# Kernel optimization log

Hardware: AMD Instinct MI355X
Metric: run time of the kernel (lower is better)

Reference implementation:

```python
import jax, jax.numpy as jnp
import numpy as np

# ---- static config (mirrors init_kwargs) ----
NS, NV, ORDER = 16, 4, 1
NUM_RBF, NUM_CH = 8, 4
C = NUM_RBF * NUM_CH              # 32 output channels per l in out_irreps
N_NODES, N_EDGES = 10000, 128000
NODE_FEAT, EDGE_FEAT = 64, 16
RDIM, RMAX = 32, 12.0
L, FC_DIM = 2, 64
# FullyConnectedTensorProduct weight numel for order=1 paths:
# (0x0->0), (0x1->1), (1x0->1), (1x1->0), (1x1->1)
WNUM = NS*NS + NS*NV + NV*NV + NV*NS + NV*NV  # 416


def _get_sorter(order, nc):
    # faithful port of TensorProductConvModel.get_sorter
    idx, orl = [], []
    for l in range(order + 1):
        for n in range(nc):
            idx.extend([n] * (2 * l + 1))
            orl.extend(range(l * l, (l + 1) * (l + 1)))
    idx, orl = np.array(idx), np.array(orl)
    return np.argsort(idx * (orl.max() + 1) + orl, kind='stable')

SORTER = jnp.asarray(_get_sorter(ORDER, C))


def _mlp(x, W1, b1, W2, b2):
    return jnp.maximum(x @ W1 + b1, 0.0) @ W2 + b2


def setup_inputs() -> dict:
    key = jax.random.key(0)
    ks = jax.random.split(key, 24)
    rn = lambda k, sh, sc: jax.random.normal(k, sh, dtype=jnp.float32) * sc
    s = lambda f: 1.0 / np.sqrt(f)
    inp = {}
    inp['pos'] = rn(ks[0], (N_NODES, 3), 3.0)
    inp['node_feats'] = rn(ks[1], (N_NODES, NODE_FEAT), 1.0)
    inp['edge_attr_in'] = rn(ks[2], (N_EDGES, EDGE_FEAT), 1.0)
    inp['edge_index'] = jax.random.randint(ks[3], (2, N_EDGES), 0, N_NODES)
    # Encoder (linear) + node_embedding MLP
    inp['enc_W'] = rn(ks[4], (NODE_FEAT, NS), s(NODE_FEAT)); inp['enc_b'] = jnp.zeros((NS,), jnp.float32)
    inp['ne_W1'] = rn(ks[5], (NS, NS), s(NS)); inp['ne_b1'] = jnp.zeros((NS,), jnp.float32)
    inp['ne_W2'] = rn(ks[6], (NS, NS), s(NS)); inp['ne_b2'] = jnp.zeros((NS,), jnp.float32)
    # edge_embedding MLP
    inp['ee_W1'] = rn(ks[7], (EDGE_FEAT, NS), s(EDGE_FEAT)); inp['ee_b1'] = jnp.zeros((NS,), jnp.float32)
    inp['ee_W2'] = rn(ks[8], (NS, NS), s(NS)); inp['ee_b2'] = jnp.zeros((NS,), jnp.float32)
    # radius_embedding MLP
    inp['re_W1'] = rn(ks[9], (RDIM, NS), s(RDIM)); inp['re_b1'] = jnp.zeros((NS,), jnp.float32)
    inp['re_W2'] = rn(ks[10], (NS, NS), s(NS)); inp['re_b2'] = jnp.zeros((NS,), jnp.float32)
    # per-layer TP edge-weight MLPs (stacked over L layers)
    inp['fc1_W'] = rn(ks[11], (L, 3 * NS, FC_DIM), s(3 * NS)); inp['fc1_b'] = jnp.zeros((L, FC_DIM), jnp.float32)
    inp['fc2_W'] = rn(ks[12], (L, FC_DIM, WNUM), s(FC_DIM)); inp['fc2_b'] = jnp.zeros((L, WNUM), jnp.float32)
    # final o3.Linear (per-l channel mixing)
    inp['lin0_W'] = rn(ks[13], (NS, C), 1.0)
    inp['lin1_W'] = rn(ks[14], (NV, C), 1.0)
    return inp


def _forward(pos, node_feats, edge_attr_in, enc_W, enc_b, ne_W1, ne_b1, ne_W2, ne_b2,
             ee_W1, ee_b1, ee_W2, ee_b2, re_W1, re_b1, re_W2, re_b2,
             fc1_W, fc1_b, fc2_W, fc2_b, lin0_W, lin1_W, edge_index):
    src, dst = edge_index[0], edge_index[1]
    N, E = pos.shape[0], src.shape[0]
    # node scalar features: Encoder -> node_embedding MLP
    h0 = _mlp(node_feats @ enc_W + enc_b, ne_W1, ne_b1, ne_W2, ne_b2)        # [N, ns]
    h1 = jnp.zeros((N, NV, 3), h0.dtype)                                      # l=1 part (zero-padded)
    # build_conv_graph (radius=False): given edges only
    edge_vec = pos[src] - pos[dst]                                            # [E, 3]
    d = jnp.linalg.norm(edge_vec, axis=-1)
    offset = jnp.linspace(0.0, RMAX, RDIM)
    coeff = -0.5 / (offset[1] - offset[0]) ** 2
    rbf = jnp.exp(coeff * (d[:, None] - offset[None, :]) ** 2)                # GaussianSmearing
    edge_attr = _mlp(edge_attr_in, ee_W1, ee_b1, ee_W2, ee_b2) + _mlp(rbf, re_W1, re_b1, re_W2, re_b2)
    # spherical harmonics, normalize=True, component normalization: Y0=1, Y1=sqrt(3)*unit
    unit = edge_vec / jnp.maximum(d, 1e-9)[:, None]
    y1 = jnp.sqrt(3.0) * unit                                                 # [E, 3]
    # scatter-mean denominators (dim_size = N)
    cnt = jnp.maximum(jax.ops.segment_sum(jnp.ones((E,), h0.dtype), src, num_segments=N), 1.0)
    a0 = 1.0 / jnp.sqrt(float(NS + NV))       # path (fan-in) norm for l=0 output
    a1 = 1.0 / jnp.sqrt(float(NS + 2 * NV))   # path norm for l=1 output
    for i in range(L):
        # edge features: [edge_attr | h0[src] | h0[dst]] -> per-edge TP weights
        ea = jnp.concatenate([edge_attr, h0[src], h0[dst]], -1)
        w = _mlp(ea, fc1_W[i], fc1_b[i], fc2_W[i], fc2_b[i])                  # [E, WNUM]
        off = 0
        w00 = w[:, off:off + NS * NS].reshape(E, NS, NS); off += NS * NS
        w011 = w[:, off:off + NS * NV].reshape(E, NS, NV); off += NS * NV
        w101 = w[:, off:off + NV * NV].reshape(E, NV, NV); off += NV * NV
        w110 = w[:, off:off + NV * NS].reshape(E, NV, NS); off += NV * NS
        w111 = w[:, off:off + NV * NV].reshape(E, NV, NV)
        x0, x1 = h0[dst], h1[dst]                                             # gather at edge_dst
        # l=0 output: (0x0->0) + (1x1->0)
        dot = jnp.einsum('enk,ek->en', x1, y1) / jnp.sqrt(3.0)
        o0 = a0 * (jnp.einsum('en,eno->eo', x0, w00) + jnp.einsum('en,eno->eo', dot, w110))
        # l=1 output: (0x1->1) + (1x0->1) + (1x1->1 cross)
        cr = jnp.cross(x1, y1[:, None, :]) / jnp.sqrt(2.0)                    # [E, nv, 3]
        o1 = a1 * (jnp.einsum('en,eno,em->eom', x0, w011, y1)
                   + jnp.einsum('enm,eno->eom', x1, w101)
                   + jnp.einsum('enm,eno->eom', cr, w111))
        # scatter-mean into edge_src, residual add
        h0 = h0 + jax.ops.segment_sum(o0, src, num_segments=N) / cnt[:, None]
        h1 = h1 + jax.ops.segment_sum(o1.reshape(E, -1), src, num_segments=N).reshape(N, NV, 3) / cnt[:, None, None]
    # final o3.Linear (per-l, fan-in normalized) -> sorter -> reshape
    f0 = (h0 @ lin0_W) / jnp.sqrt(float(NS))                                   # [N, C]
    f1 = jnp.einsum('nvm,vc->ncm', h1, lin1_W) / jnp.sqrt(float(NV))           # [N, C, 3]
    flat = jnp.concatenate([f0, f1.reshape(N, C * 3)], -1)                     # irreps-flat layout
    return flat[:, SORTER].reshape(N, NUM_CH, NUM_RBF, (ORDER + 1) ** 2)


def reference(pos, node_feats, edge_attr_in, edge_index, enc_W, enc_b, ne_W1, ne_b1, ne_W2, ne_b2,
              ee_W1, ee_b1, ee_W2, ee_b2, re_W1, re_b1, re_W2, re_b2,
              fc1_W, fc1_b, fc2_W, fc2_b, lin0_W, lin1_W):
    return _forward(pos, node_feats, edge_attr_in, enc_W, enc_b, ne_W1, ne_b1, ne_W2, ne_b2,
                    ee_W1, ee_b1, ee_W2, ee_b2, re_W1, re_b1, re_W2, re_b2,
                    fc1_W, fc1_b, fc2_W, fc2_b, lin0_W, lin1_W, edge_index)
```

## Files before the change

kernel.cpp:

```cpp
#include <hip/hip_runtime.h>
#include <math.h>

#define SQRT3f     1.7320508075688772f
#define INV_SQRT3f 0.5773502691896258f
#define INV_SQRT2f 0.7071067811865476f
#define A0f        0.22360679774997896f
#define A1f        0.20412414523193150f

typedef __attribute__((ext_vector_type(8))) short bf16x8;
typedef __attribute__((ext_vector_type(4))) float f32x4;

__device__ __forceinline__ float4 ld4(const float* p) {
    return *reinterpret_cast<const float4*>(p);
}

__device__ __forceinline__ unsigned short f2bf(float x) {
    unsigned int u = __float_as_uint(x);
    u = (u + 0x7FFFu + ((u >> 16) & 1u)) >> 16;
    return (unsigned short)u;
}
__device__ __forceinline__ float bf2f(unsigned short u) {
    return __uint_as_float(((unsigned int)u) << 16);
}
__device__ __forceinline__ unsigned int pk2(float a, float b) {
    return (unsigned int)f2bf(a) | ((unsigned int)f2bf(b) << 16);
}
__device__ __forceinline__ float bflo(unsigned int u) {
    return __uint_as_float(u << 16);
}
__device__ __forceinline__ float bfhi(unsigned int u) {
    return __uint_as_float(u & 0xFFFF0000u);
}
__device__ __forceinline__ float pick4(uint2 v, int r) {
    return (r == 0) ? bflo(v.x) : (r == 1) ? bfhi(v.x)
         : (r == 2) ? bflo(v.y) : bfhi(v.y);
}

template<bool RELU>
__device__ __forceinline__ void mm16x16(const float* in, const float* W,
                                        const float* b, float* out)
{
#pragma unroll
    for (int t = 0; t < 16; ++t) out[t] = b[t];
#pragma unroll
    for (int s = 0; s < 16; ++s) {
        float a = in[s];
#pragma unroll
        for (int q = 0; q < 4; ++q) {
            float4 w = *reinterpret_cast<const float4*>(W + s * 16 + q * 4);
            out[q*4+0] += a * w.x; out[q*4+1] += a * w.y;
            out[q*4+2] += a * w.z; out[q*4+3] += a * w.w;
        }
    }
    if (RELU) {
#pragma unroll
        for (int t = 0; t < 16; ++t) out[t] = fmaxf(out[t], 0.f);
    }
}

__global__ __launch_bounds__(256)
void embed_hist_pack_kernel(const float* __restrict__ nf,
                            const float* __restrict__ encW, const float* __restrict__ encb,
                            const float* __restrict__ neW1, const float* __restrict__ neb1,
                            const float* __restrict__ neW2, const float* __restrict__ neb2,
                            float* __restrict__ h0, int N,
                            const int* __restrict__ srcI, int* __restrict__ cntI, int E,
                            const float* __restrict__ fc2W, const float* __restrict__ fc1W,
                            unsigned short* __restrict__ w2p, unsigned short* __restrict__ w1p,
                            int nblkA, int nblkB)
{
    int tid = threadIdx.x;
    int bid = (int)blockIdx.x;
    if (bid >= nblkA + nblkB) {
        int idx = (bid - nblkA - nblkB) * 256 + tid;
        const int NW2 = 2 * 26 * 2 * 64;
        if (idx < NW2) {
            int lane  = idx & 63;
            int ks    = (idx >> 6) & 1;
            int nt    = (idx >> 7) % 26;
            int layer = idx / (26 * 2 * 64);
            const float* W = fc2W + (size_t)layer * 64 * 416;
            unsigned short* out = w2p + (size_t)layer * 26 * 2 * 64 * 8
                                      + (size_t)((nt * 2 + ks) * 64 + lane) * 8;
            int k0 = ks * 32 + (lane >> 4) * 8;
            int c  = nt * 16 + (lane & 15);
#pragma unroll
            for (int j = 0; j < 8; ++j) out[j] = f2bf(W[(size_t)(k0 + j) * 416 + c]);
        } else {
            int i2 = idx - NW2;
            if (i2 >= 2 * 4 * 2 * 64) return;
            int lane  = i2 & 63;
            int ks    = (i2 >> 6) & 1;
            int nt    = (i2 >> 7) & 3;
            int layer = i2 >> 9;
            const float* W = fc1W + (size_t)layer * 48 * 64;
            unsigned short* out = w1p + (size_t)(((layer * 4 + nt) * 2 + ks) * 64 + lane) * 8;
            int k0 = ks * 32 + (lane >> 4) * 8;
            int n  = nt * 16 + (lane & 15);
#pragma unroll
            for (int j = 0; j < 8; ++j) {
                int k = k0 + j;
                out[j] = (k < 48) ? f2bf(W[(size_t)k * 64 + n]) : (unsigned short)0;
            }
        }
        return;
    }
    if (bid >= nblkA) {
        int e = (bid - nblkA) * 256 + tid;
        if (e < E) atomicAdd(&cntI[srcI[e]], 1);
        return;
    }
    __shared__ float encWs[1024];
    __shared__ float neW1s[256];
    __shared__ float neW2s[256];
    __shared__ float bs[48];
    for (int i = tid; i < 1024; i += 256) encWs[i] = encW[i];
    neW1s[tid] = neW1[tid];
    neW2s[tid] = neW2[tid];
    if (tid < 16)      bs[tid] = encb[tid];
    else if (tid < 32) bs[tid] = neb1[tid - 16];
    else if (tid < 48) bs[tid] = neb2[tid - 32];
    __syncthreads();

    int n = bid * 256 + tid;
    if (n >= N) return;
    float x[16];
#pragma unroll
    for (int s = 0; s < 16; ++s) x[s] = bs[s];
    for (int i = 0; i < 64; ++i) {
        float a = nf[(size_t)n * 64 + i];
#pragma unroll
        for (int q = 0; q < 4; ++q) {
            float4 w = *reinterpret_cast<const float4*>(&encWs[i * 16 + q * 4]);
            x[q*4+0] += a * w.x; x[q*4+1] += a * w.y;
            x[q*4+2] += a * w.z; x[q*4+3] += a * w.w;
        }
    }
    float h[16], o[16];
    mm16x16<true >(x, neW1s, bs + 16, h);
    mm16x16<false>(h, neW2s, bs + 32, o);
#pragma unroll
    for (int j = 0; j < 16; ++j) h0[(size_t)n * 16 + j] = o[j];
}

__global__ __launch_bounds__(1024)
void scan_kernel(const int* __restrict__ cntI, int* __restrict__ start,
                 int* __restrict__ cursor, float* __restrict__ invcnt, int N)
{
    __shared__ int wsum[16];
    __shared__ int ctot;
    int tid = threadIdx.x;
    int lane = tid & 63, wid = tid >> 6;
    int run = 0;
    for (int c0 = 0; c0 < N; c0 += 1024) {
        int i = c0 + tid;
        int v = (i < N) ? cntI[i] : 0;
        int x = v;
#pragma unroll
        for (int off = 1; off < 64; off <<= 1) {
            int y = __shfl_up(x, off);
            if (lane >= off) x += y;
        }
        if (lane == 63) wsum[wid] = x;
        __syncthreads();
        if (wid == 0) {
            int w = (lane < 16) ? wsum[lane] : 0;
#pragma unroll
            for (int off = 1; off < 16; off <<= 1) {
                int y = __shfl_up(w, off);
                if (lane >= off) w += y;
            }
            if (lane < 16) wsum[lane] = w;
            if (lane == 15) ctot = w;
        }
        __syncthreads();
        int base = (wid > 0) ? wsum[wid - 1] : 0;
        int incl = x + base;
        if (i < N) {
            int st = run + incl - v;
            start[i] = st;
            cursor[i] = st;
            invcnt[i] = 1.0f / fmaxf((float)v, 1.0f);
        }
        run += ctot;
        __syncthreads();
    }
}

__global__ __launch_bounds__(256)
void edge_pre_kernel(const float* __restrict__ pos, const float* __restrict__ eain,
                     const int* __restrict__ srcI, const int* __restrict__ dstI,
                     int* __restrict__ cursor,
                     const float* __restrict__ eeW1, const float* __restrict__ eeb1,
                     const float* __restrict__ eeW2, const float* __restrict__ eeb2,
                     const float* __restrict__ reW1, const float* __restrict__ reb1,
                     const float* __restrict__ reW2, const float* __restrict__ reb2,
                     float* __restrict__ eattr, float* __restrict__ y1s,
                     int* __restrict__ srcS, int* __restrict__ dstS, int E)
{
    __shared__ float ws_[1280];
    __shared__ float bs_[64];
    float* eeW1s = ws_;
    float* eeW2s = ws_ + 256;
    float* reW1s = ws_ + 512;
    float* reW2s = ws_ + 1024;
    int tid = threadIdx.x;
    eeW1s[tid] = eeW1[tid];
    eeW2s[tid] = eeW2[tid];
    reW1s[tid] = reW1[tid];
    reW1s[tid + 256] = reW1[tid + 256];
    reW2s[tid] = reW2[tid];
    if (tid < 16)      bs_[tid] = eeb1[tid];
    else if (tid < 32) bs_[tid] = eeb2[tid - 16];
    else if (tid < 48) bs_[tid] = reb1[tid - 32];
    else if (tid < 64) bs_[tid] = reb2[tid - 48];
    __syncthreads();

    int e = blockIdx.x * blockDim.x + tid;
    if (e >= E) return;
    int s = srcI[e], d = dstI[e];
    int p = atomicAdd(&cursor[s], 1);
    srcS[p] = s; dstS[p] = d;
    float vx = pos[s*3+0] - pos[d*3+0];
    float vy = pos[s*3+1] - pos[d*3+1];
    float vz = pos[s*3+2] - pos[d*3+2];
    float dist = sqrtf(vx*vx + vy*vy + vz*vz);
    float inv = 1.f / fmaxf(dist, 1e-9f);
    y1s[(size_t)p*3+0] = SQRT3f * vx * inv;
    y1s[(size_t)p*3+1] = SQRT3f * vy * inv;
    y1s[(size_t)p*3+2] = SQRT3f * vz * inv;

    const float step  = 12.0f / 31.0f;
    const float coeff = -0.5f / (step * step);
    float rbf[32];
#pragma unroll
    for (int j = 0; j < 32; ++j) {
        float t = dist - (float)j * step;
        rbf[j] = expf(coeff * t * t);
    }

    float ein[16];
#pragma unroll
    for (int j = 0; j < 16; ++j) ein[j] = eain[(size_t)e * 16 + j];

    float t1[16], a1v[16];
    mm16x16<true >(ein, eeW1s, bs_, t1);
    mm16x16<false>(t1, eeW2s, bs_ + 16, a1v);

    float t2[16];
#pragma unroll
    for (int t = 0; t < 16; ++t) t2[t] = bs_[32 + t];
#pragma unroll
    for (int j = 0; j < 32; ++j) {
        float a = rbf[j];
#pragma unroll
        for (int q = 0; q < 4; ++q) {
            float4 w = *reinterpret_cast<const float4*>(&reW1s[j * 16 + q * 4]);
            t2[q*4+0] += a * w.x; t2[q*4+1] += a * w.y;
            t2[q*4+2] += a * w.z; t2[q*4+3] += a * w.w;
        }
    }
#pragma unroll
    for (int t = 0; t < 16; ++t) t2[t] = fmaxf(t2[t], 0.f);
    float a2v[16];
    mm16x16<false>(t2, reW2s, bs_ + 48, a2v);

#pragma unroll
    for (int j = 0; j < 16; ++j) eattr[(size_t)p * 16 + j] = a1v[j] + a2v[j];
}

template<bool HAS_L1>
__global__ __launch_bounds__(256)
void fused_tp_kernel(const float* __restrict__ h0, const float* __restrict__ h1,
                     const float* __restrict__ eattr, const float* __restrict__ y1s,
                     const int* __restrict__ srcS, const int* __restrict__ dstS,
                     const unsigned short* __restrict__ w1p, const float* __restrict__ b1,
                     const unsigned short* __restrict__ w2p, const float* __restrict__ b2,
                     float* __restrict__ oo0, float* __restrict__ oo1, int E)
{
    __shared__ unsigned short eas[128 * 64];
    __shared__ unsigned short x0sT[16 * 128];
    __shared__ unsigned short x1sT[12 * 128];
    __shared__ unsigned short dotsT[4 * 128];
    __shared__ unsigned short crsT[12 * 128];
    __shared__ unsigned short y1lT[3 * 128];

    int tid = threadIdx.x;
    int ebase = blockIdx.x * 128;

    {
        int lx = tid & 127;
        int half = tid >> 7;
        int p = ebase + lx;
        int sw = lx & 7;
        uint4 pk;
        if (half == 0) {
            float4 va = ld4(eattr + (size_t)p * 16 + 0);
            float4 vb = ld4(eattr + (size_t)p * 16 + 4);
            float4 vc = ld4(eattr + (size_t)p * 16 + 8);
            float4 vd = ld4(eattr + (size_t)p * 16 + 12);
            pk.x = pk2(va.x, va.y); pk.y = pk2(va.z, va.w);
            pk.z = pk2(vb.x, vb.y); pk.w = pk2(vb.z, vb.w);
            *reinterpret_cast<uint4*>(&eas[lx * 64 + ((0 ^ sw) << 3)]) = pk;
            pk.x = pk2(vc.x, vc.y); pk.y = pk2(vc.z, vc.w);
            pk.z = pk2(vd.x, vd.y); pk.w = pk2(vd.z, vd.w);
            *reinterpret_cast<uint4*>(&eas[lx * 64 + ((1 ^ sw) << 3)]) = pk;

            int s = srcS[p];
            va = ld4(h0 + (size_t)s * 16 + 0); vb = ld4(h0 + (size_t)s * 16 + 4);
            vc = ld4(h0 + (size_t)s * 16 + 8); vd = ld4(h0 + (size_t)s * 16 + 12);
            pk.x = pk2(va.x, va.y); pk.y = pk2(va.z, va.w);
            pk.z = pk2(vb.x, vb.y); pk.w = pk2(vb.z, vb.w);
            *reinterpret_cast<uint4*>(&eas[lx * 64 + ((2 ^ sw) << 3)]) = pk;
            pk.x = pk2(vc.x, vc.y); pk.y = pk2(vc.z, vc.w);
            pk.z = pk2(vd.x, vd.y); pk.w = pk2(vd.z, vd.w);
            *reinterpret_cast<uint4*>(&eas[lx * 64 + ((3 ^ sw) << 3)]) = pk;
        } else {
            int d = dstS[p];
            float4 va = ld4(h0 + (size_t)d * 16 + 0);
            float4 vb = ld4(h0 + (size_t)d * 16 + 4);
            float4 vc = ld4(h0 + (size_t)d * 16 + 8);
            float4 vd = ld4(h0 + (size_t)d * 16 + 12);
            pk.x = pk2(va.x, va.y); pk.y = pk2(va.z, va.w);
            pk.z = pk2(vb.x, vb.y); pk.w = pk2(vb.z, vb.w);
            *reinterpret_cast<uint4*>(&eas[lx * 64 + ((4 ^ sw) << 3)]) = pk;
            pk.x = pk2(vc.x, vc.y); pk.y = pk2(vc.z, vc.w);
            pk.z = pk2(vd.x, vd.y); pk.w = pk2(vd.z, vd.w);
            *reinterpret_cast<uint4*>(&eas[lx * 64 + ((5 ^ sw) << 3)]) = pk;
            uint4 z = {0u, 0u, 0u, 0u};
            *reinterpret_cast<uint4*>(&eas[lx * 64 + ((6 ^ sw) << 3)]) = z;
            *reinterpret_cast<uint4*>(&eas[lx * 64 + ((7 ^ sw) << 3)]) = z;

            x0sT[ 0*128+lx]=f2bf(va.x); x0sT[ 1*128+lx]=f2bf(va.y);
            x0sT[ 2*128+lx]=f2bf(va.z); x0sT[ 3*128+lx]=f2bf(va.w);
            x0sT[ 4*128+lx]=f2bf(vb.x); x0sT[ 5*128+lx]=f2bf(vb.y);
            x0sT[ 6*128+lx]=f2bf(vb.z); x0sT[ 7*128+lx]=f2bf(vb.w);
            x0sT[ 8*128+lx]=f2bf(vc.x); x0sT[ 9*128+lx]=f2bf(vc.y);
            x0sT[10*128+lx]=f2bf(vc.z); x0sT[11*128+lx]=f2bf(vc.w);
            x0sT[12*128+lx]=f2bf(vd.x); x0sT[13*128+lx]=f2bf(vd.y);
            x0sT[14*128+lx]=f2bf(vd.z); x0sT[15*128+lx]=f2bf(vd.w);

            float yv0 = y1s[(size_t)p*3+0], yv1 = y1s[(size_t)p*3+1], yv2 = y1s[(size_t)p*3+2];
            y1lT[0*128+lx] = f2bf(yv0);
            y1lT[1*128+lx] = f2bf(yv1);
            y1lT[2*128+lx] = f2bf(yv2);

            if (HAS_L1) {
#pragma unroll
                for (int v = 0; v < 4; ++v) {
                    float xa = h1[(size_t)d*12 + v*3 + 0];
                    float xb = h1[(size_t)d*12 + v*3 + 1];
                    float xc = h1[(size_t)d*12 + v*3 + 2];
                    x1sT[(v*3+0)*128+lx] = f2bf(xa);
                    x1sT[(v*3+1)*128+lx] = f2bf(xb);
                    x1sT[(v*3+2)*128+lx] = f2bf(xc);
                    dotsT[v*128+lx] = f2bf((xa*yv0 + xb*yv1 + xc*yv2) * INV_SQRT3f);
                    crsT[(v*3+0)*128+lx] = f2bf((xb*yv2 - xc*yv1) * INV_SQRT2f);
                    crsT[(v*3+1)*128+lx] = f2bf((xc*yv0 - xa*yv2) * INV_SQRT2f);
                    crsT[(v*3+2)*128+lx] = f2bf((xa*yv1 - xb*yv0) * INV_SQRT2f);
                }
            }
        }
    }
    __syncthreads();

    int wave = tid >> 6;
    int lane = tid & 63;
    int col = lane & 15;
    int grp = lane >> 4;
    int mrow0 = wave * 32;

    {
        bf16x8 a1[2][2];
#pragma unroll
        for (int m = 0; m < 2; ++m) {
            int row = mrow0 + m * 16 + col;
            int r7 = row & 7;
#pragma unroll
            for (int ks = 0; ks < 2; ++ks) {
                int kc = grp + ks * 4;
                a1[m][ks] = *reinterpret_cast<const bf16x8*>(
                    &eas[row * 64 + ((kc ^ r7) << 3)]);
            }
        }
        f32x4 hacc[4][2];
#pragma unroll
        for (int nt = 0; nt < 4; ++nt) {
            const bf16x8* bp = reinterpret_cast<const bf16x8*>(
                w1p + (size_t)((nt * 2) * 64 + lane) * 8);
            bf16x8 b0 = bp[0];
            bf16x8 b1f = bp[64];
            float bs = b1[nt * 16 + col];
            f32x4 cin = {bs, bs, bs, bs};
#pragma unroll
            for (int m = 0; m < 2; ++m) {
                f32x4 acc = cin;
                acc = __builtin_amdgcn_mfma_f32_16x16x32_bf16(a1[m][0], b0, acc, 0, 0, 0);
                acc = __builtin_amdgcn_mfma_f32_16x16x32_bf16(a1[m][1], b1f, acc, 0, 0, 0);
                hacc[nt][m] = acc;
            }
        }
#pragma unroll
        for (int nt = 0; nt < 4; ++nt) {
            int chunkbase = nt * 2 + (col >> 3);
            int cw = col & 7;
#pragma unroll
            for (int m = 0; m < 2; ++m) {
#pragma unroll
                for (int r = 0; r < 4; ++r) {
                    int edge = mrow0 + m * 16 + grp * 4 + r;
                    unsigned short hv = f2bf(fmaxf(hacc[nt][m][r], 0.f));
                    eas[edge * 64 + ((chunkbase ^ (edge & 7)) << 3) + cw] = hv;
                }
            }
        }
    }

    asm volatile("s_waitcnt lgkmcnt(0)" ::: "memory");
    __builtin_amdgcn_sched_barrier(0);

    bf16x8 a[2][2];
#pragma unroll
    for (int m = 0; m < 2; ++m) {
        int row = mrow0 + m * 16 + col;
        int r7 = row & 7;
        a[m][0] = *reinterpret_cast<const bf16x8*>(&eas[row * 64 + ((grp ^ r7) << 3)]);
        a[m][1] = *reinterpret_cast<const bf16x8*>(&eas[row * 64 + (((grp + 4) ^ r7) << 3)]);
    }

    float o0a[2][4];
    float t011p[2][4];
    float o1p[2][4][3];
#pragma unroll
    for (int m = 0; m < 2; ++m)
#pragma unroll
        for (int r = 0; r < 4; ++r) {
            o0a[m][r] = 0.f; t011p[m][r] = 0.f;
            o1p[m][r][0] = 0.f; o1p[m][r][1] = 0.f; o1p[m][r][2] = 0.f;
        }

    const int NT = HAS_L1 ? 26 : 20;
    for (int nt = 0; nt < NT; ++nt) {
        const bf16x8* bp = reinterpret_cast<const bf16x8*>(
            w2p + (size_t)(nt * 2 * 64 + lane) * 8);
        bf16x8 b0 = bp[0];
        bf16x8 b1f = bp[64];
        float bias = b2[nt * 16 + col];
        f32x4 cin = {bias, bias, bias, bias};
#pragma unroll
        for (int m = 0; m < 2; ++m) {
            f32x4 acc = cin;
            acc = __builtin_amdgcn_mfma_f32_16x16x32_bf16(a[m][0], b0, acc, 0, 0, 0);
            acc = __builtin_amdgcn_mfma_f32_16x16x32_bf16(a[m][1], b1f, acc, 0, 0, 0);
            int lx0 = mrow0 + m * 16 + grp * 4;
            if (nt < 16) {
                uint2 xv = *reinterpret_cast<const uint2*>(&x0sT[nt * 128 + lx0]);
#pragma unroll
                for (int r = 0; r < 4; ++r)
                    o0a[m][r] += pick4(xv, r) * acc[r];
            } else if (nt < 20) {
                int n = (nt - 16) * 4 + (col >> 2);
                uint2 xv = *reinterpret_cast<const uint2*>(&x0sT[n * 128 + lx0]);
#pragma unroll
                for (int r = 0; r < 4; ++r)
                    t011p[m][r] += pick4(xv, r) * acc[r];
            } else if (nt == 20) {
                int n = col >> 2;
#pragma unroll
                for (int d = 0; d < 3; ++d) {
                    uint2 xv = *reinterpret_cast<const uint2*>(&x1sT[(n * 3 + d) * 128 + lx0]);
#pragma unroll
                    for (int r = 0; r < 4; ++r)
                        o1p[m][r][d] += pick4(xv, r) * acc[r];
                }
            } else if (nt < 25) {
                int n = nt - 21;
                uint2 xv = *reinterpret_cast<const uint2*>(&dotsT[n * 128 + lx0]);
#pragma unroll
                for (int r = 0; r < 4; ++r)
                    o0a[m][r] += pick4(xv, r) * acc[r];
            } else {
                int n = col >> 2;
#pragma unroll
                for (int d = 0; d < 3; ++d) {
                    uint2 xv = *reinterpret_cast<const uint2*>(&crsT[(n * 3 + d) * 128 + lx0]);
#pragma unroll
                    for (int r = 0; r < 4; ++r)
                        o1p[m][r][d] += pick4(xv, r) * acc[r];
                }
            }
        }
    }

#pragma unroll
    for (int m = 0; m < 2; ++m) {
        int lx0 = mrow0 + m * 16 + grp * 4;
        uint2 yv0 = *reinterpret_cast<const uint2*>(&y1lT[0 * 128 + lx0]);
        uint2 yv1 = *reinterpret_cast<const uint2*>(&y1lT[1 * 128 + lx0]);
        uint2 yv2 = *reinterpret_cast<const uint2*>(&y1lT[2 * 128 + lx0]);
#pragma unroll
        for (int r = 0; r < 4; ++r) {
            int lx = lx0 + r;
            size_t e = (size_t)(ebase + lx);
            float t = t011p[m][r];
            t += __shfl_xor(t, 4);
            t += __shfl_xor(t, 8);
            float yr[3] = {pick4(yv0, r), pick4(yv1, r), pick4(yv2, r)};
            float o1v[3];
#pragma unroll
            for (int d = 0; d < 3; ++d) {
                float v = o1p[m][r][d];
                v += __shfl_xor(v, 4);
                v += __shfl_xor(v, 8);
                o1v[d] = v + t * yr[d];
            }
            oo0[e * 16 + col] = A0f * o0a[m][r];
            if (col < 4) {
#pragma unroll
                for (int d = 0; d < 3; ++d)
                    oo1[e * 12 + col * 3 + d] = A1f * o1v[d];
            }
        }
    }
}

template<bool FINAL>
__global__ __launch_bounds__(256)
void node_update_kernel(float* __restrict__ h0, float* __restrict__ h1,
                        const float* __restrict__ oo0, const float* __restrict__ oo1,
                        const int* __restrict__ start, const int* __restrict__ cntI,
                        const float* __restrict__ invcnt,
                        const float* __restrict__ lin0, const float* __restrict__ lin1,
                        float* __restrict__ out, int N)
{
    __shared__ float lin0s[512];
    __shared__ float lin1s[128];
    __shared__ float hh0[32][16];
    __shared__ float hh1[32][12];

    int tx = threadIdx.x;
    int ty = threadIdx.y;
    int tid = ty * 8 + tx;
    if (FINAL) {
        lin0s[tid] = lin0[tid];
        lin0s[tid + 256] = lin0[tid + 256];
        if (tid < 128) lin1s[tid] = lin1[tid];
    }

    int n = blockIdx.x * 32 + ty;
    if (n < N) {
        int p0 = start[n], c = cntI[n];
        float4 acc = {0.f, 0.f, 0.f, 0.f};
        if (tx < 4) {
            for (int k = 0; k < c; ++k) {
                float4 v = ld4(oo0 + (size_t)(p0 + k) * 16 + tx * 4);
                acc.x += v.x; acc.y += v.y; acc.z += v.z; acc.w += v.w;
            }
        } else if (tx < 7) {
            for (int k = 0; k < c; ++k) {
                float4 v = ld4(oo1 + (size_t)(p0 + k) * 12 + (tx - 4) * 4);
                acc.x += v.x; acc.y += v.y; acc.z += v.z; acc.w += v.w;
            }
        }
        float invc = invcnt[n];
        if (tx < 4) {
            float4 h = ld4(h0 + (size_t)n * 16 + tx * 4);
            h.x += acc.x * invc; h.y += acc.y * invc;
            h.z += acc.z * invc; h.w += acc.w * invc;
            if (FINAL) {
                hh0[ty][tx*4+0] = h.x; hh0[ty][tx*4+1] = h.y;
                hh0[ty][tx*4+2] = h.z; hh0[ty][tx*4+3] = h.w;
            } else {
                *reinterpret_cast<float4*>(h0 + (size_t)n * 16 + tx * 4) = h;
            }
        } else if (tx < 7) {
            float4 h = ld4(h1 + (size_t)n * 12 + (tx - 4) * 4);
            h.x += acc.x * invc; h.y += acc.y * invc;
            h.z += acc.z * invc; h.w += acc.w * invc;
            if (FINAL) {
                hh1[ty][(tx-4)*4+0] = h.x; hh1[ty][(tx-4)*4+1] = h.y;
                hh1[ty][(tx-4)*4+2] = h.z; hh1[ty][(tx-4)*4+3] = h.w;
            } else {
                *reinterpret_cast<float4*>(h1 + (size_t)n * 12 + (tx - 4) * 4) = h;
            }
        }
    }
    if (FINAL) {
        __syncthreads();
        if (n >= N) return;
#pragma unroll
        for (int q = 0; q < 4; ++q) {
            int c = tx * 4 + q;
            float f0 = 0.f;
#pragma unroll
            for (int s = 0; s < 16; ++s) f0 += hh0[ty][s] * lin0s[s * 32 + c];
            float f1x = 0.f, f1y = 0.f, f1z = 0.f;
#pragma unroll
            for (int v = 0; v < 4; ++v) {
                float w = lin1s[v * 32 + c];
                f1x += hh1[ty][v * 3 + 0] * w;
                f1y += hh1[ty][v * 3 + 1] * w;
                f1z += hh1[ty][v * 3 + 2] * w;
            }
            float4 r;
            r.x = f0 * 0.25f;
            r.y = f1x * 0.5f;
            r.z = f1y * 0.5f;
            r.w = f1z * 0.5f;
            *reinterpret_cast<float4*>(out + (size_t)n * 128 + c * 4) = r;
        }
    }
}

extern "C" void kernel_launch(void* const* d_in, const int* in_sizes, int n_in,
                              void* d_out, int out_size, void* d_ws, size_t ws_size,
                              hipStream_t stream)
{
    const float* pos  = (const float*)d_in[0];
    const float* nf   = (const float*)d_in[1];
    const float* eain = (const float*)d_in[2];
    const int*   eidx = (const int*)  d_in[3];
    const float* encW = (const float*)d_in[4];
    const float* encb = (const float*)d_in[5];
    const float* neW1 = (const float*)d_in[6];
    const float* neb1 = (const float*)d_in[7];
    const float* neW2 = (const float*)d_in[8];
    const float* neb2 = (const float*)d_in[9];
    const float* eeW1 = (const float*)d_in[10];
    const float* eeb1 = (const float*)d_in[11];
    const float* eeW2 = (const float*)d_in[12];
    const float* eeb2 = (const float*)d_in[13];
    const float* reW1 = (const float*)d_in[14];
    const float* reb1 = (const float*)d_in[15];
    const float* reW2 = (const float*)d_in[16];
    const float* reb2 = (const float*)d_in[17];
    const float* fc1W = (const float*)d_in[18];
    const float* fc1b = (const float*)d_in[19];
    const float* fc2W = (const float*)d_in[20];
    const float* fc2b = (const float*)d_in[21];
    const float* lin0 = (const float*)d_in[22];
    const float* lin1 = (const float*)d_in[23];

    int N = in_sizes[0] / 3;
    int E = in_sizes[3] / 2;
    const int* srcI = eidx;
    const int* dstI = eidx + E;

    float* ws = (float*)d_ws;
    size_t o = 0;
    float* h0     = ws + o; o += (size_t)N * 16;
    float* h1     = ws + o; o += (size_t)N * 12;
    float* eat    = ws + o; o += (size_t)E * 16;
    float* y1s    = ws + o; o += (size_t)E * 3;
    float* oo0    = ws + o; o += (size_t)E * 16;
    float* oo1    = ws + o; o += (size_t)E * 12;
    float* invcnt = ws + o; o += (size_t)N;
    int* cntI   = (int*)(ws + o); o += (size_t)N;
    int* startA = (int*)(ws + o); o += (size_t)N;
    int* cursor = (int*)(ws + o); o += (size_t)N;
    int* srcS   = (int*)(ws + o); o += (size_t)E;
    int* dstS   = (int*)(ws + o); o += (size_t)E;
    unsigned short* w2p = (unsigned short*)(ws + o); o += 2 * 26 * 2 * 64 * 8 / 2;
    unsigned short* w1p = (unsigned short*)(ws + o); o += 2 * 4 * 2 * 64 * 8 / 2;

    hipMemsetAsync(h1,   0, sizeof(float) * (size_t)N * 12, stream);
    hipMemsetAsync(cntI, 0, sizeof(int) * (size_t)N, stream);

    int nblkA = (N + 255) / 256;
    int nblkB = (E + 255) / 256;
    embed_hist_pack_kernel<<<nblkA + nblkB + 30, 256, 0, stream>>>(
        nf, encW, encb, neW1, neb1, neW2, neb2, h0, N, srcI, cntI, E,
        fc2W, fc1W, w2p, w1p, nblkA, nblkB);

    scan_kernel<<<1, 1024, 0, stream>>>(cntI, startA, cursor, invcnt, N);

    edge_pre_kernel<<<nblkB, 256, 0, stream>>>(
        pos, eain, srcI, dstI, cursor, eeW1, eeb1, eeW2, eeb2,
        reW1, reb1, reW2, reb2, eat, y1s, srcS, dstS, E);

    dim3 nub(8, 32);
    int nublk = (N + 31) / 32;
    for (int i = 0; i < 2; ++i) {
        const float* fb1 = fc1b + (size_t)i * 64;
        const float* fb2 = fc2b + (size_t)i * 416;
        const unsigned short* w1pi = w1p + (size_t)i * 4 * 2 * 64 * 8;
        const unsigned short* w2pi = w2p + (size_t)i * 26 * 2 * 64 * 8;
        if (i == 0) {
            fused_tp_kernel<false><<<E / 128, 256, 0, stream>>>(
                h0, h1, eat, y1s, srcS, dstS, w1pi, fb1, w2pi, fb2, oo0, oo1, E);
            node_update_kernel<false><<<nublk, nub, 0, stream>>>(
                h0, h1, oo0, oo1, startA, cntI, invcnt, lin0, lin1, (float*)d_out, N);
        } else {
            fused_tp_kernel<true><<<E / 128, 256, 0, stream>>>(
                h0, h1, eat, y1s, srcS, dstS, w1pi, fb1, w2pi, fb2, oo0, oo1, E);
            node_update_kernel<true><<<nublk, nub, 0, stream>>>(
                h0, h1, oo0, oo1, startA, cntI, invcnt, lin0, lin1, (float*)d_out, N);
        }
    }
}
```

Before: 256.3 us.

## Use 512 threads per block in fused TP kernel, one 16-row tile per wave

Doubles the fused tensor-product block from 256 to 512 threads, so each of 8 waves handles one 16-edge MFMA tile instead of two. The shared-memory staging is split four ways (edge attrs, src features, dst features, y1/L1 products) so gathers run in parallel across more threads. The aim is more latency hiding and fewer serial MFMA/accumulate steps per wave. In exchange, each wave reloads the same B weight fragments for half the work, which doubles weight-load traffic per edge. The dst index is also reloaded in the last quarter.

```diff
diff --git a/kernel.cpp b/kernel.cpp
--- a/kernel.cpp
+++ b/kernel.cpp
@@ -270,7 +270,7 @@
 }
 
 template<bool HAS_L1>
-__global__ __launch_bounds__(256)
+__global__ __launch_bounds__(512)
 void fused_tp_kernel(const float* __restrict__ h0, const float* __restrict__ h1,
                      const float* __restrict__ eattr, const float* __restrict__ y1s,
                      const int* __restrict__ srcS, const int* __restrict__ dstS,
@@ -290,11 +290,11 @@
 
     {
         int lx = tid & 127;
-        int half = tid >> 7;
+        int q = tid >> 7;
         int p = ebase + lx;
         int sw = lx & 7;
         uint4 pk;
-        if (half == 0) {
+        if (q == 0) {
             float4 va = ld4(eattr + (size_t)p * 16 + 0);
             float4 vb = ld4(eattr + (size_t)p * 16 + 4);
             float4 vc = ld4(eattr + (size_t)p * 16 + 8);
@@ -305,17 +305,19 @@
             pk.x = pk2(vc.x, vc.y); pk.y = pk2(vc.z, vc.w);
             pk.z = pk2(vd.x, vd.y); pk.w = pk2(vd.z, vd.w);
             *reinterpret_cast<uint4*>(&eas[lx * 64 + ((1 ^ sw) << 3)]) = pk;
-
+        } else if (q == 1) {
             int s = srcS[p];
-            va = ld4(h0 + (size_t)s * 16 + 0); vb = ld4(h0 + (size_t)s * 16 + 4);
-            vc = ld4(h0 + (size_t)s * 16 + 8); vd = ld4(h0 + (size_t)s * 16 + 12);
+            float4 va = ld4(h0 + (size_t)s * 16 + 0);
+            float4 vb = ld4(h0 + (size_t)s * 16 + 4);
+            float4 vc = ld4(h0 + (size_t)s * 16 + 8);
+            float4 vd = ld4(h0 + (size_t)s * 16 + 12);
             pk.x = pk2(va.x, va.y); pk.y = pk2(va.z, va.w);
             pk.z = pk2(vb.x, vb.y); pk.w = pk2(vb.z, vb.w);
             *reinterpret_cast<uint4*>(&eas[lx * 64 + ((2 ^ sw) << 3)]) = pk;
             pk.x = pk2(vc.x, vc.y); pk.y = pk2(vc.z, vc.w);
             pk.z = pk2(vd.x, vd.y); pk.w = pk2(vd.z, vd.w);
             *reinterpret_cast<uint4*>(&eas[lx * 64 + ((3 ^ sw) << 3)]) = pk;
-        } else {
+        } else if (q == 2) {
             int d = dstS[p];
             float4 va = ld4(h0 + (size_t)d * 16 + 0);
             float4 vb = ld4(h0 + (size_t)d * 16 + 4);
@@ -327,9 +329,6 @@
             pk.x = pk2(vc.x, vc.y); pk.y = pk2(vc.z, vc.w);
             pk.z = pk2(vd.x, vd.y); pk.w = pk2(vd.z, vd.w);
             *reinterpret_cast<uint4*>(&eas[lx * 64 + ((5 ^ sw) << 3)]) = pk;
-            uint4 z = {0u, 0u, 0u, 0u};
-            *reinterpret_cast<uint4*>(&eas[lx * 64 + ((6 ^ sw) << 3)]) = z;
-            *reinterpret_cast<uint4*>(&eas[lx * 64 + ((7 ^ sw) << 3)]) = z;
 
             x0sT[ 0*128+lx]=f2bf(va.x); x0sT[ 1*128+lx]=f2bf(va.y);
             x0sT[ 2*128+lx]=f2bf(va.z); x0sT[ 3*128+lx]=f2bf(va.w);
@@ -339,6 +338,10 @@
             x0sT[10*128+lx]=f2bf(vc.z); x0sT[11*128+lx]=f2bf(vc.w);
             x0sT[12*128+lx]=f2bf(vd.x); x0sT[13*128+lx]=f2bf(vd.y);
             x0sT[14*128+lx]=f2bf(vd.z); x0sT[15*128+lx]=f2bf(vd.w);
+        } else {
+            uint4 z = {0u, 0u, 0u, 0u};
+            *reinterpret_cast<uint4*>(&eas[lx * 64 + ((6 ^ sw) << 3)]) = z;
+            *reinterpret_cast<uint4*>(&eas[lx * 64 + ((7 ^ sw) << 3)]) = z;
 
             float yv0 = y1s[(size_t)p*3+0], yv1 = y1s[(size_t)p*3+1], yv2 = y1s[(size_t)p*3+2];
             y1lT[0*128+lx] = f2bf(yv0);
@@ -346,6 +349,7 @@
             y1lT[2*128+lx] = f2bf(yv2);
 
             if (HAS_L1) {
+                int d = dstS[p];
 #pragma unroll
                 for (int v = 0; v < 4; ++v) {
                     float xa = h1[(size_t)d*12 + v*3 + 0];
@@ -368,22 +372,17 @@
     int lane = tid & 63;
     int col = lane & 15;
     int grp = lane >> 4;
-    int mrow0 = wave * 32;
+    int mrow0 = wave * 16;
 
     {
-        bf16x8 a1[2][2];
-#pragma unroll
-        for (int m = 0; m < 2; ++m) {
-            int row = mrow0 + m * 16 + col;
+        bf16x8 a1[2];
+        {
+            int row = mrow0 + col;
             int r7 = row & 7;
-#pragma unroll
-            for (int ks = 0; ks < 2; ++ks) {
-                int kc = grp + ks * 4;
-                a1[m][ks] = *reinterpret_cast<const bf16x8*>(
-                    &eas[row * 64 + ((kc ^ r7) << 3)]);
-            }
-        }
-        f32x4 hacc[4][2];
+            a1[0] = *reinterpret_cast<const bf16x8*>(&eas[row * 64 + ((grp ^ r7) << 3)]);
+            a1[1] = *reinterpret_cast<const bf16x8*>(&eas[row * 64 + (((grp + 4) ^ r7) << 3)]);
+        }
+        f32x4 hacc[4];
 #pragma unroll
         for (int nt = 0; nt < 4; ++nt) {
             const bf16x8* bp = reinterpret_cast<const bf16x8*>(
@@ -391,27 +390,20 @@
             bf16x8 b0 = bp[0];
             bf16x8 b1f = bp[64];
             float bs = b1[nt * 16 + col];
-            f32x4 cin = {bs, bs, bs, bs};
-#pragma unroll
-            for (int m = 0; m < 2; ++m) {
-                f32x4 acc = cin;
-                acc = __builtin_amdgcn_mfma_f32_16x16x32_bf16(a1[m][0], b0, acc, 0, 0, 0);
-                acc = __builtin_amdgcn_mfma_f32_16x16x32_bf16(a1[m][1], b1f, acc, 0, 0, 0);
-                hacc[nt][m] = acc;
-            }
+            f32x4 acc = {bs, bs, bs, bs};
+            acc = __builtin_amdgcn_mfma_f32_16x16x32_bf16(a1[0], b0, acc, 0, 0, 0);
+            acc = __builtin_amdgcn_mfma_f32_16x16x32_bf16(a1[1], b1f, acc, 0, 0, 0);
+            hacc[nt] = acc;
         }
 #pragma unroll
         for (int nt = 0; nt < 4; ++nt) {
             int chunkbase = nt * 2 + (col >> 3);
             int cw = col & 7;
 #pragma unroll
-            for (int m = 0; m < 2; ++m) {
-#pragma unroll
-                for (int r = 0; r < 4; ++r) {
-                    int edge = mrow0 + m * 16 + grp * 4 + r;
-                    unsigned short hv = f2bf(fmaxf(hacc[nt][m][r], 0.f));
-                    eas[edge * 64 + ((chunkbase ^ (edge & 7)) << 3) + cw] = hv;
-                }
+            for (int r = 0; r < 4; ++r) {
+                int edge = mrow0 + grp * 4 + r;
+                unsigned short hv = f2bf(fmaxf(hacc[nt][r], 0.f));
+                eas[edge * 64 + ((chunkbase ^ (edge & 7)) << 3) + cw] = hv;
             }
         }
     }
@@ -419,26 +411,24 @@
     asm volatile("s_waitcnt lgkmcnt(0)" ::: "memory");
     __builtin_amdgcn_sched_barrier(0);
 
-    bf16x8 a[2][2];
-#pragma unroll
-    for (int m = 0; m < 2; ++m) {
-        int row = mrow0 + m * 16 + col;
+    bf16x8 a[2];
+    {
+        int row = mrow0 + col;
         int r7 = row & 7;
-        a[m][0] = *reinterpret_cast<const bf16x8*>(&eas[row * 64 + ((grp ^ r7) << 3)]);
-        a[m][1] = *reinterpret_cast<const bf16x8*>(&eas[row * 64 + (((grp + 4) ^ r7) << 3)]);
-    }
-
-    float o0a[2][4];
-    float t011p[2][4];
-    float o1p[2][4][3];
-#pragma unroll
-    for (int m = 0; m < 2; ++m)
-#pragma unroll
-        for (int r = 0; r < 4; ++r) {
-            o0a[m][r] = 0.f; t011p[m][r] = 0.f;
-            o1p[m][r][0] = 0.f; o1p[m][r][1] = 0.f; o1p[m][r][2] = 0.f;
-        }
-
+        a[0] = *reinterpret_cast<const bf16x8*>(&eas[row * 64 + ((grp ^ r7) << 3)]);
+        a[1] = *reinterpret_cast<const bf16x8*>(&eas[row * 64 + (((grp + 4) ^ r7) << 3)]);
+    }
+
+    float o0a[4];
+    float t011p[4];
+    float o1p[4][3];
+#pragma unroll
+    for (int r = 0; r < 4; ++r) {
+        o0a[r] = 0.f; t011p[r] = 0.f;
+        o1p[r][0] = 0.f; o1p[r][1] = 0.f; o1p[r][2] = 0.f;
+    }
+
+    int lx0 = mrow0 + grp * 4;
     const int NT = HAS_L1 ? 26 : 20;
     for (int nt = 0; nt < NT; ++nt) {
         const bf16x8* bp = reinterpret_cast<const bf16x8*>(
@@ -446,55 +436,48 @@
         bf16x8 b0 = bp[0];
         bf16x8 b1f = bp[64];
         float bias = b2[nt * 16 + col];
-        f32x4 cin = {bias, bias, bias, bias};
-#pragma unroll
-        for (int m = 0; m < 2; ++m) {
-            f32x4 acc = cin;
-            acc = __builtin_amdgcn_mfma_f32_16x16x32_bf16(a[m][0], b0, acc, 0, 0, 0);
-            acc = __builtin_amdgcn_mfma_f32_16x16x32_bf16(a[m][1], b1f, acc, 0, 0, 0);
-            int lx0 = mrow0 + m * 16 + grp * 4;
-            if (nt < 16) {
-                uint2 xv = *reinterpret_cast<const uint2*>(&x0sT[nt * 128 + lx0]);
+        f32x4 acc = {bias, bias, bias, bias};
+        acc = __builtin_amdgcn_mfma_f32_16x16x32_bf16(a[0], b0, acc, 0, 0, 0);
+        acc = __builtin_amdgcn_mfma_f32_16x16x32_bf16(a[1], b1f, acc, 0, 0, 0);
+        if (nt < 16) {
+            uint2 xv = *reinterpret_cast<const uint2*>(&x0sT[nt * 128 + lx0]);
+#pragma unroll
+            for (int r = 0; r < 4; ++r)
+                o0a[r] += pick4(xv, r) * acc[r];
+        } else if (nt < 20) {
+            int n = (nt - 16) * 4 + (col >> 2);
+            uint2 xv = *reinterpret_cast<const uint2*>(&x0sT[n * 128 + lx0]);
+#pragma unroll
+            for (int r = 0; r < 4; ++r)
+                t011p[r] += pick4(xv, r) * acc[r];
+        } else if (nt == 20) {
+            int n = col >> 2;
+#pragma unroll
+            for (int d = 0; d < 3; ++d) {
+                uint2 xv = *reinterpret_cast<const uint2*>(&x1sT[(n * 3 + d) * 128 + lx0]);
 #pragma unroll
                 for (int r = 0; r < 4; ++r)
-                    o0a[m][r] += pick4(xv, r) * acc[r];
-            } else if (nt < 20) {
-                int n = (nt - 16) * 4 + (col >> 2);
-                uint2 xv = *reinterpret_cast<const uint2*>(&x0sT[n * 128 + lx0]);
+                    o1p[r][d] += pick4(xv, r) * acc[r];
+            }
+        } else if (nt < 25) {
+            int n = nt - 21;
+            uint2 xv = *reinterpret_cast<const uint2*>(&dotsT[n * 128 + lx0]);
+#pragma unroll
+            for (int r = 0; r < 4; ++r)
+                o0a[r] += pick4(xv, r) * acc[r];
+        } else {
+            int n = col >> 2;
+#pragma unroll
+            for (int d = 0; d < 3; ++d) {
+                uint2 xv = *reinterpret_cast<const uint2*>(&crsT[(n * 3 + d) * 128 + lx0]);
 #pragma unroll
                 for (int r = 0; r < 4; ++r)
-                    t011p[m][r] += pick4(xv, r) * acc[r];
-            } else if (nt == 20) {
-                int n = col >> 2;
-#pragma unroll
-                for (int d = 0; d < 3; ++d) {
-                    uint2 xv = *reinterpret_cast<const uint2*>(&x1sT[(n * 3 + d) * 128 + lx0]);
-#pragma unroll
-                    for (int r = 0; r < 4; ++r)
-                        o1p[m][r][d] += pick4(xv, r) * acc[r];
-                }
-            } else if (nt < 25) {
-                int n = nt - 21;
-                uint2 xv = *reinterpret_cast<const uint2*>(&dotsT[n * 128 + lx0]);
-#pragma unroll
-                for (int r = 0; r < 4; ++r)
-                    o0a[m][r] += pick4(xv, r) * acc[r];
-            } else {
-                int n = col >> 2;
-#pragma unroll
-                for (int d = 0; d < 3; ++d) {
-                    uint2 xv = *reinterpret_cast<const uint2*>(&crsT[(n * 3 + d) * 128 + lx0]);
-#pragma unroll
-                    for (int r = 0; r < 4; ++r)
-                        o1p[m][r][d] += pick4(xv, r) * acc[r];
-                }
-            }
-        }
-    }
-
-#pragma unroll
-    for (int m = 0; m < 2; ++m) {
-        int lx0 = mrow0 + m * 16 + grp * 4;
+                    o1p[r][d] += pick4(xv, r) * acc[r];
+            }
+        }
+    }
+
+    {
         uint2 yv0 = *reinterpret_cast<const uint2*>(&y1lT[0 * 128 + lx0]);
         uint2 yv1 = *reinterpret_cast<const uint2*>(&y1lT[1 * 128 + lx0]);
         uint2 yv2 = *reinterpret_cast<const uint2*>(&y1lT[2 * 128 + lx0]);
@@ -502,19 +485,19 @@
         for (int r = 0; r < 4; ++r) {
             int lx = lx0 + r;
             size_t e = (size_t)(ebase + lx);
-            float t = t011p[m][r];
+            float t = t011p[r];
             t += __shfl_xor(t, 4);
             t += __shfl_xor(t, 8);
             float yr[3] = {pick4(yv0, r), pick4(yv1, r), pick4(yv2, r)};
             float o1v[3];
 #pragma unroll
             for (int d = 0; d < 3; ++d) {
-                float v = o1p[m][r][d];
+                float v = o1p[r][d];
                 v += __shfl_xor(v, 4);
                 v += __shfl_xor(v, 8);
                 o1v[d] = v + t * yr[d];
             }
-            oo0[e * 16 + col] = A0f * o0a[m][r];
+            oo0[e * 16 + col] = A0f * o0a[r];
             if (col < 4) {
 #pragma unroll
                 for (int d = 0; d < 3; ++d)
@@ -686,12 +669,12 @@
         const unsigned short* w1pi = w1p + (size_t)i * 4 * 2 * 64 * 8;
         const unsigned short* w2pi = w2p + (size_t)i * 26 * 2 * 64 * 8;
         if (i == 0) {
-            fused_tp_kernel<false><<<E / 128, 256, 0, stream>>>(
+            fused_tp_kernel<false><<<E / 128, 512, 0, stream>>>(
                 h0, h1, eat, y1s, srcS, dstS, w1pi, fb1, w2pi, fb2, oo0, oo1, E);
             node_update_kernel<false><<<nublk, nub, 0, stream>>>(
                 h0, h1, oo0, oo1, startA, cntI, invcnt, lin0, lin1, (float*)d_out, N);
         } else {
-            fused_tp_kernel<true><<<E / 128, 256, 0, stream>>>(
+            fused_tp_kernel<true><<<E / 128, 512, 0, stream>>>(
                 h0, h1, eat, y1s, srcS, dstS, w1pi, fb1, w2pi, fb2, oo0, oo1, E);
             node_update_kernel<true><<<nublk, nub, 0, stream>>>(
                 h0, h1, oo0, oo1, startA, cntI, invcnt, lin0, lin1, (float*)d_out, N);
```

New measurement: 262.6 us. +2.4%, slower.
